# Kernel tuning notes

Measured on AMD Instinct MI355X. Metric: run time of the kernel, lower is better.

## Reference

```python
import jax, jax.numpy as jnp
import numpy as np

B, S, D = 4, 4096, 256


def _complex_linear(x_r, x_i, w_r, w_i):
    # torch nn.Linear: y = x @ W.T ; complex mult: (Wr + i Wi)(xr + i xi)
    real = x_r @ w_r.T - x_i @ w_i.T
    imag = x_i @ w_r.T + x_r @ w_i.T
    return real, imag


def setup_inputs() -> dict:
    key = jax.random.key(0)
    ks = jax.random.split(key, 8)
    std = 1.0 / np.sqrt(D)  # ~ nn.Linear default init scale
    return {
        "query_real": jax.random.normal(ks[0], (B, S, D), jnp.float32),
        "query_imag": jax.random.normal(ks[1], (B, S, D), jnp.float32),
        "wq_real": jax.random.normal(ks[2], (D, D), jnp.float32) * std,
        "wq_imag": jax.random.normal(ks[3], (D, D), jnp.float32) * std,
        "wk_real": jax.random.normal(ks[4], (D, D), jnp.float32) * std,
        "wk_imag": jax.random.normal(ks[5], (D, D), jnp.float32) * std,
        "wv_real": jax.random.normal(ks[6], (D, D), jnp.float32) * std,
        "wv_imag": jax.random.normal(ks[7], (D, D), jnp.float32) * std,
    }


def reference(query_real, query_imag, wq_real, wq_imag, wk_real, wk_imag, wv_real, wv_imag):
    dim = query_real.shape[-1]
    scale = dim ** (-0.5)  # faithful: uses dim, not 2*dim

    q_r, q_i = _complex_linear(query_real, query_imag, wq_real, wq_imag)
    k_r, k_i = _complex_linear(query_real, query_imag, wk_real, wk_imag)
    v_r, v_i = _complex_linear(query_real, query_imag, wv_real, wv_imag)

    q_flat = jnp.concatenate([q_r, q_i], axis=-1)  # [B,S,2D]
    k_flat = jnp.concatenate([k_r, k_i], axis=-1)  # [B,S,2D]

    scores = jnp.einsum('bqd,bkd->bqk', q_flat, k_flat) * scale  # [B,S,S]
    attn = jax.nn.softmax(scores, axis=-1)

    out_r = jnp.einsum('bqk,bkd->bqd', attn, v_r)
    out_i = jnp.einsum('bqk,bkd->bqd', attn, v_i)
    return out_r, out_i, attn
```

## Files before the change

### kernel.cpp

```cpp
#include <hip/hip_runtime.h>
#include <hip/hip_fp16.h>

typedef _Float16 f16;
typedef _Float16 f16x8 __attribute__((ext_vector_type(8)));
typedef _Float16 f16x4 __attribute__((ext_vector_type(4)));
typedef float f32x4 __attribute__((ext_vector_type(4)));

#define AS1 __attribute__((address_space(1)))
#define AS3 __attribute__((address_space(3)))

__device__ __forceinline__ void g2l16(const void* g, void* l) {
  __builtin_amdgcn_global_load_lds((const AS1 void*)g, (AS3 void*)l, 16, 0, 0);
}

__device__ __forceinline__ void xcd_swz(int& bx, int& by, int& bz) {
  int gx = gridDim.x, gy = gridDim.y;
  int nwg = gx * gy * gridDim.z;
  int lin = (blockIdx.z * gy + blockIdx.y) * gx + blockIdx.x;
  int swz = (lin & 7) * (nwg >> 3) + (lin >> 3);
  bx = swz % gx;
  int t = swz / gx;
  by = t % gy;
  bz = t / gy;
}

__global__ __launch_bounds__(256) void build_x(const float* __restrict__ qr,
                                               const float* __restrict__ qi,
                                               f16* __restrict__ X) {
  long i = (long)blockIdx.x * 256 + threadIdx.x;
  long e = i * 4;
  int m = (int)(e >> 9);
  int k = (int)(e & 511);
  const float* src = (k < 256) ? (qr + (long)m * 256 + k)
                               : (qi + (long)m * 256 + (k - 256));
  float4 v = *(const float4*)src;
  f16x4 h = {(f16)v.x, (f16)v.y, (f16)v.z, (f16)v.w};
  *(f16x4*)(X + e) = h;
}

__global__ __launch_bounds__(256) void build_w(const float* __restrict__ wqr,
                                               const float* __restrict__ wqi,
                                               const float* __restrict__ wkr,
                                               const float* __restrict__ wki,
                                               const float* __restrict__ wvr,
                                               const float* __restrict__ wvi,
                                               f16* __restrict__ W) {
  long i = (long)blockIdx.x * 256 + threadIdx.x;
  long e = i * 4;
  int n = (int)(e >> 9);
  int k = (int)(e & 511);
  int sel = n >> 8;
  int row = n & 255;
  int k2 = k & 255;
  bool hi = (k >= 256);
  const float *Wr, *Wi;
  if ((sel >> 1) == 0)      { Wr = wqr; Wi = wqi; }
  else if ((sel >> 1) == 1) { Wr = wkr; Wi = wki; }
  else                      { Wr = wvr; Wi = wvi; }
  const float* src;
  float sgn = 1.0f;
  if ((sel & 1) == 0) {
    if (!hi) src = Wr + (long)row * 256 + k2;
    else   { src = Wi + (long)row * 256 + k2; sgn = -1.0f; }
  } else {
    if (!hi) src = Wi + (long)row * 256 + k2;
    else     src = Wr + (long)row * 256 + k2;
  }
  float4 v = *(const float4*)src;
  f16x4 h = {(f16)(sgn * v.x), (f16)(sgn * v.y), (f16)(sgn * v.z), (f16)(sgn * v.w)};
  *(f16x4*)(W + e) = h;
}

template <int MODE>
__global__ __launch_bounds__(512, 4) void gemm_nt(const f16* __restrict__ A, int lda, long astr,
                                                  const f16* __restrict__ B, int ldb, long bstr,
                                                  int K, float scale,
                                                  void* __restrict__ C0, long cstr,
                                                  float2* __restrict__ stats) {
  __shared__ __align__(16) f16 As[256 * 64];
  __shared__ __align__(16) f16 Bs[128 * 64];
  int bx, by, bz;
  xcd_swz(bx, by, bz);
  const f16* Ab = A + (long)bz * astr;
  const f16* Bb = B + (long)bz * bstr;
  const int tid = threadIdx.x;
  const int wave = tid >> 6, lane = tid & 63;
  const int bm = by * 256, bn = bx * 128;
  const int wm = (wave >> 1) * 64, wn = (wave & 1) * 64;
  const int lr = lane & 15, lg = lane >> 4;

  const int srow = wave * 8 + (lane >> 3);
  const int sk = ((lane & 7) ^ (lane >> 3)) * 8;

  f32x4 acc[4][4] = {};

  for (int kt = 0; kt < K; kt += 64) {
#pragma unroll
    for (int it = 0; it < 4; ++it)
      g2l16(Ab + (long)(bm + srow + it * 64) * lda + kt + sk,
            (char*)As + it * 8192 + wave * 1024);
#pragma unroll
    for (int it = 0; it < 2; ++it)
      g2l16(Bb + (long)(bn + srow + it * 64) * ldb + kt + sk,
            (char*)Bs + it * 8192 + wave * 1024);
    __syncthreads();
#pragma unroll
    for (int kk = 0; kk < 2; ++kk) {
      f16x8 af[4], bf[4];
#pragma unroll
      for (int f = 0; f < 4; ++f) {
        int sw = ((kk * 4 + lg) ^ (lr & 7)) * 8;
        af[f] = *(const f16x8*)(As + (wm + f * 16 + lr) * 64 + sw);
        bf[f] = *(const f16x8*)(Bs + (wn + f * 16 + lr) * 64 + sw);
      }
#pragma unroll
      for (int fm = 0; fm < 4; ++fm)
#pragma unroll
        for (int fn = 0; fn < 4; ++fn)
          acc[fm][fn] = __builtin_amdgcn_mfma_f32_16x16x32_f16(af[fm], bf[fn], acc[fm][fn], 0, 0, 0);
    }
    __syncthreads();
  }

#pragma unroll
  for (int fm = 0; fm < 4; ++fm) {
#pragma unroll
    for (int fn = 0; fn < 4; ++fn) {
#pragma unroll
      for (int r = 0; r < 4; ++r) {
        int row = bm + wm + fm * 16 + lg * 4 + r;
        int col = bn + wn + fn * 16 + lr;
        float v = acc[fm][fn][r];
        if (MODE == 0) {
          ((f16*)C0)[(long)row * 1536 + col] = (f16)v;
        } else {
          ((f16*)C0)[(long)bz * cstr + (long)row * 4096 + col] = (f16)(v * scale);
        }
      }
    }
  }

  if (MODE == 1) {
    const int nt = bx * 2 + (wn >> 6);
#pragma unroll
    for (int fm = 0; fm < 4; ++fm) {
#pragma unroll
      for (int r = 0; r < 4; ++r) {
        float v0 = acc[fm][0][r] * scale, v1 = acc[fm][1][r] * scale;
        float v2 = acc[fm][2][r] * scale, v3 = acc[fm][3][r] * scale;
        float mt = fmaxf(fmaxf(v0, v1), fmaxf(v2, v3));
#pragma unroll
        for (int off = 8; off >= 1; off >>= 1) mt = fmaxf(mt, __shfl_xor(mt, off));
        float lt = __expf(v0 - mt) + __expf(v1 - mt) + __expf(v2 - mt) + __expf(v3 - mt);
#pragma unroll
        for (int off = 8; off >= 1; off >>= 1) lt += __shfl_xor(lt, off);
        if (lr == 0) {
          int row = bm + wm + fm * 16 + lg * 4 + r;
          stats[(long)nt * 16384 + (long)bz * 4096 + row] = make_float2(mt, lt);
        }
      }
    }
  }
}

__global__ __launch_bounds__(256) void build_vt(const f16* __restrict__ P,
                                                f16* __restrict__ VT) {
  __shared__ f16 t[64][66];
  const int tid = threadIdx.x;
  const long b = blockIdx.z;
  const f16* src = P + (b * 4096 + (long)blockIdx.x * 64) * 1536 + 1024 + blockIdx.y * 64;
#pragma unroll
  for (int it = 0; it < 16; ++it) {
    int lin = it * 256 + tid;
    int i = lin >> 6, j = lin & 63;
    t[i][j] = src[(long)i * 1536 + j];
  }
  __syncthreads();
  f16* dst = VT + (b * 512 + (long)blockIdx.y * 64) * 4096 + blockIdx.x * 64;
#pragma unroll
  for (int it = 0; it < 16; ++it) {
    int lin = it * 256 + tid;
    int i = lin >> 6, j = lin & 63;
    dst[(long)i * 4096 + j] = t[j][i];
  }
}

__global__ __launch_bounds__(256) void merge_stats(const float2* __restrict__ stats,
                                                   float2* __restrict__ ml) {
  long row = (long)blockIdx.x * 256 + threadIdx.x;
  float m = -1e30f;
#pragma unroll 8
  for (int i = 0; i < 64; ++i) m = fmaxf(m, stats[i * 16384 + row].x);
  float l = 0.0f;
#pragma unroll 8
  for (int i = 0; i < 64; ++i) {
    float2 s = stats[i * 16384 + row];
    l += s.y * __expf(s.x - m);
  }
  ml[row] = make_float2(m, l);
}

__global__ __launch_bounds__(512) void pv_fused4(const float2* __restrict__ ml,
                                                 const f16* __restrict__ S16,
                                                 const f16* __restrict__ VT,
                                                 float* __restrict__ attn,
                                                 float* __restrict__ outR,
                                                 float* __restrict__ outI) {
  __shared__ __align__(16) f16 Ps0[64 * 64];
  __shared__ __align__(16) f16 Ps1[64 * 64];
  __shared__ __align__(16) f16 Ps2[64 * 64];
  __shared__ __align__(16) f16 Bs0[256 * 64];
  __shared__ __align__(16) f16 Bs1[256 * 64];
  __shared__ __align__(16) f16 Bs2[256 * 64];
  int lin = blockIdx.x;
  int swz = (lin & 7) * 64 + (lin >> 3);
  int b = swz >> 7;
  int rem = swz & 127;
  int rt = rem >> 1, ch = rem & 1;
  const int bm = rt * 64;
  const int c0 = ch * 256;

  const int tid = threadIdx.x;
  const int wave = tid >> 6, lane = tid & 63;
  const int wm2 = (wave >> 2) * 32;
  const int wn2 = (wave & 3) * 64;
  const int lr = lane & 15, lg = lane >> 4;

  const int prow = tid >> 3;
  const int pc8 = tid & 7;
  const int vrow = wave * 8 + (lane >> 3);
  const int vsw = ((lane & 7) ^ ((lane >> 3) & 7)) * 8;
  float2 mlv = ml[(long)b * 4096 + bm + prow];
  const float mrow = mlv.x;
  const float invl = 1.0f / mlv.y;

  const f16* Sb = S16 + ((long)(b * 4096 + bm + prow)) * 4096 + pc8 * 8;
  float* Ab = attn + ((long)(b * 4096 + bm + prow)) * 4096 + pc8 * 8;
  const f16* Vb = VT + (long)(b * 512 + c0) * 4096;
  const int pslot = (pc8 ^ (prow & 7)) * 8;

  f32x4 acc[2][4] = {};
  f16x8 s0, s1, s2, sini;

#define PV_G2L(BSBUF, KT)                                                   \
  {                                                                         \
    _Pragma("unroll")                                                       \
    for (int i = 0; i < 4; ++i)                                             \
      g2l16(Vb + (long)(i * 64 + vrow) * 4096 + (KT) + vsw,                 \
            (char*)BSBUF + i * 8192 + wave * 1024);                         \
  }

#define PV_EXP(SC, PSBUF, KT, PAR)                                          \
  {                                                                         \
    float p[8];                                                             \
    _Pragma("unroll") for (int j = 0; j < 8; ++j)                           \
      p[j] = __expf((float)SC[j] - mrow) * invl;                            \
    if ((PAR) == ch) {                                                      \
      float4 w0 = {p[0], p[1], p[2], p[3]};                                 \
      float4 w1 = {p[4], p[5], p[6], p[7]};                                 \
      *(float4*)(Ab + (KT)) = w0;                                           \
      *(float4*)(Ab + (KT) + 4) = w1;                                       \
    }                                                                       \
    f16x8 h = {(f16)p[0], (f16)p[1], (f16)p[2], (f16)p[3],                  \
               (f16)p[4], (f16)p[5], (f16)p[6], (f16)p[7]};                 \
    *(f16x8*)(PSBUF + prow * 64 + pslot) = h;                               \
  }

#define PV_MFMA(PSBUF, BSBUF)                                               \
  {                                                                         \
    __builtin_amdgcn_s_setprio(1);                                          \
    _Pragma("unroll")                                                       \
    for (int kk = 0; kk < 2; ++kk) {                                        \
      f16x8 af[2];                                                          \
      _Pragma("unroll")                                                     \
      for (int fm = 0; fm < 2; ++fm)                                        \
        af[fm] = *(const f16x8*)(PSBUF + (wm2 + fm * 16 + lr) * 64 +        \
                                 ((kk * 4 + lg) ^ (lr & 7)) * 8);           \
      f16x8 bf[4];                                                          \
      _Pragma("unroll")                                                     \
      for (int f = 0; f < 4; ++f)                                           \
        bf[f] = *(const f16x8*)(BSBUF + (wn2 + f * 16 + lr) * 64 +          \
                                ((kk * 4 + lg) ^ (lr & 7)) * 8);            \
      _Pragma("unroll")                                                     \
      for (int fm = 0; fm < 2; ++fm)                                        \
        _Pragma("unroll")                                                   \
        for (int f = 0; f < 4; ++f)                                         \
          acc[fm][f] = __builtin_amdgcn_mfma_f32_16x16x32_f16(              \
              af[fm], bf[f], acc[fm][f], 0, 0, 0);                          \
    }                                                                       \
    __builtin_amdgcn_s_setprio(0);                                          \
  }

#define PV_SYNC(N)                                                          \
  asm volatile("s_waitcnt vmcnt(" #N ")" ::: "memory");                     \
  asm volatile("s_waitcnt lgkmcnt(0)" ::: "memory");                        \
  __builtin_amdgcn_s_barrier();                                             \
  __builtin_amdgcn_sched_barrier(0);

#define PV_TILE(T, BCUR, BPRE, PCUR, PNXT, SCONS, SLOAD)                    \
  {                                                                         \
    PV_G2L(BPRE, ((T) + 2) * 64)                                            \
    SLOAD = *(const f16x8*)(Sb + ((T) + 3) * 64);                           \
    PV_EXP(SCONS, PNXT, ((T) + 1) * 64, (((T) + 1) & 1))                    \
    PV_MFMA(PCUR, BCUR)                                                     \
    PV_SYNC(8)                                                              \
  }

  PV_G2L(Bs0, 0)
  PV_G2L(Bs1, 64)
  sini = *(const f16x8*)(Sb + 0);
  s1 = *(const f16x8*)(Sb + 64);
  s2 = *(const f16x8*)(Sb + 128);
  PV_EXP(sini, Ps0, 0, 0)
  PV_SYNC(7)

  for (int tb = 0; tb < 60; tb += 6) {
    PV_TILE(tb + 0, Bs0, Bs2, Ps0, Ps1, s1, s0)
    PV_TILE(tb + 1, Bs1, Bs0, Ps1, Ps2, s2, s1)
    PV_TILE(tb + 2, Bs2, Bs1, Ps2, Ps0, s0, s2)
    PV_TILE(tb + 3, Bs0, Bs2, Ps0, Ps1, s1, s0)
    PV_TILE(tb + 4, Bs1, Bs0, Ps1, Ps2, s2, s1)
    PV_TILE(tb + 5, Bs2, Bs1, Ps2, Ps0, s0, s2)
  }

  {
    PV_G2L(Bs2, 62 * 64)
    s0 = *(const f16x8*)(Sb + 63 * 64);
    PV_EXP(s1, Ps1, 61 * 64, 1)
    PV_MFMA(Ps0, Bs0)
    PV_SYNC(8)
  }
  {
    PV_G2L(Bs0, 63 * 64)
    PV_EXP(s2, Ps2, 62 * 64, 0)
    PV_MFMA(Ps1, Bs1)
    PV_SYNC(7)
  }
  {
    PV_EXP(s0, Ps0, 63 * 64, 1)
    PV_MFMA(Ps2, Bs2)
    PV_SYNC(2)
  }
  PV_MFMA(Ps0, Bs0)

#undef PV_TILE
#undef PV_SYNC
#undef PV_MFMA
#undef PV_EXP
#undef PV_G2L

  float* outp = ch ? outI : outR;
#pragma unroll
  for (int fm = 0; fm < 2; ++fm)
#pragma unroll
    for (int f = 0; f < 4; ++f)
#pragma unroll
      for (int r = 0; r < 4; ++r) {
        int row = bm + wm2 + fm * 16 + lg * 4 + r;
        int col = wn2 + f * 16 + lr;
        outp[((long)b * 4096 + row) * 256 + col] = acc[fm][f][r];
      }
}

extern "C" void kernel_launch(void* const* d_in, const int* in_sizes, int n_in,
                              void* d_out, int out_size, void* d_ws, size_t ws_size,
                              hipStream_t stream) {
  const float* qr  = (const float*)d_in[0];
  const float* qi  = (const float*)d_in[1];
  const float* wqr = (const float*)d_in[2];
  const float* wqi = (const float*)d_in[3];
  const float* wkr = (const float*)d_in[4];
  const float* wki = (const float*)d_in[5];
  const float* wvr = (const float*)d_in[6];
  const float* wvi = (const float*)d_in[7];

  float* outR = (float*)d_out;
  float* outI = outR + (size_t)4 * 4096 * 256;
  float* attn = outI + (size_t)4 * 4096 * 256;

  const size_t offX  = 0;
  const size_t offW  = offX + (size_t)16384 * 512 * 2;
  const size_t offP  = offW + (size_t)1536 * 512 * 2;
  const size_t offVT = offP + (size_t)16384 * 1536 * 2;
  const size_t offS  = offVT + (size_t)4 * 512 * 4096 * 2;

  char* ws = (char*)d_ws;
  f16* X   = (f16*)(ws + offX);
  f16* W   = (f16*)(ws + offW);
  f16* P   = (f16*)(ws + offP);
  f16* VT  = (f16*)(ws + offVT);
  f16* S16 = (f16*)(ws + offS);
  float2* stats = (float2*)X;
  float2* ml    = (float2*)W;

  build_x<<<8192, 256, 0, stream>>>(qr, qi, X);
  build_w<<<768, 256, 0, stream>>>(wqr, wqi, wkr, wki, wvr, wvi, W);

  gemm_nt<0><<<dim3(12, 64, 1), 512, 0, stream>>>(X, 512, 0L, W, 512, 0L, 512, 1.0f,
                                                  (void*)P, 0L, nullptr);

  build_vt<<<dim3(64, 8, 4), 256, 0, stream>>>(P, VT);

  gemm_nt<1><<<dim3(32, 16, 4), 512, 0, stream>>>(P, 1536, (long)4096 * 1536,
                                                  P + 512, 1536, (long)4096 * 1536,
                                                  512, 0.0625f,
                                                  (void*)S16, (long)4096 * 4096, stats);

  merge_stats<<<64, 256, 0, stream>>>(stats, ml);

  pv_fused4<<<512, 512, 0, stream>>>(ml, S16, VT, attn, outR, outI);
}
```

Before: 367.7 us.

## Compute softmax probabilities directly in MFMA A-fragment registers, skipping LDS staging

Replaces the PV kernel so each wave loads S16 scores straight into the register layout the MFMA A operand expects, exponentiates and normalizes them in registers, and feeds them to the MFMA without writing P into shared memory. Tiles become 128 rows by 128 output columns, with a double-buffered V tile in LDS and a launch bound hint for higher occupancy. Only the first column block writes the fp32 attention matrix, converting from the f16 fragments, so attn values now carry f16 rounding. This removes the LDS round trip and the P-tile barrier dependency, but each score is reloaded and exponentiated four times (once per column block) instead of twice.

```diff
diff --git a/kernel.cpp b/kernel.cpp
--- a/kernel.cpp
+++ b/kernel.cpp
@@ -200,166 +200,178 @@
   ml[row] = make_float2(m, l);
 }
 
-__global__ __launch_bounds__(512) void pv_fused4(const float2* __restrict__ ml,
-                                                 const f16* __restrict__ S16,
-                                                 const f16* __restrict__ VT,
-                                                 float* __restrict__ attn,
-                                                 float* __restrict__ outR,
-                                                 float* __restrict__ outI) {
-  __shared__ __align__(16) f16 Ps0[64 * 64];
-  __shared__ __align__(16) f16 Ps1[64 * 64];
-  __shared__ __align__(16) f16 Ps2[64 * 64];
-  __shared__ __align__(16) f16 Bs0[256 * 64];
-  __shared__ __align__(16) f16 Bs1[256 * 64];
-  __shared__ __align__(16) f16 Bs2[256 * 64];
+__global__ __launch_bounds__(512, 4) void pv_direct(const float2* __restrict__ ml,
+                                                    const f16* __restrict__ S16,
+                                                    const f16* __restrict__ VT,
+                                                    float* __restrict__ attn,
+                                                    float* __restrict__ outR,
+                                                    float* __restrict__ outI) {
+  __shared__ __align__(16) f16 Bs0[128 * 64];
+  __shared__ __align__(16) f16 Bs1[128 * 64];
   int lin = blockIdx.x;
   int swz = (lin & 7) * 64 + (lin >> 3);
+  int cb = swz & 3;
+  int rt = (swz >> 2) & 31;
   int b = swz >> 7;
-  int rem = swz & 127;
-  int rt = rem >> 1, ch = rem & 1;
-  const int bm = rt * 64;
-  const int c0 = ch * 256;
+  const int bm = rt * 128;
 
   const int tid = threadIdx.x;
   const int wave = tid >> 6, lane = tid & 63;
-  const int wm2 = (wave >> 2) * 32;
-  const int wn2 = (wave & 3) * 64;
+  const int wm3 = (wave >> 1) * 32;
+  const int wn3 = (wave & 1) * 64;
+  const int kkw = wave & 1;
   const int lr = lane & 15, lg = lane >> 4;
 
-  const int prow = tid >> 3;
-  const int pc8 = tid & 7;
   const int vrow = wave * 8 + (lane >> 3);
   const int vsw = ((lane & 7) ^ ((lane >> 3) & 7)) * 8;
-  float2 mlv = ml[(long)b * 4096 + bm + prow];
-  const float mrow = mlv.x;
-  const float invl = 1.0f / mlv.y;
-
-  const f16* Sb = S16 + ((long)(b * 4096 + bm + prow)) * 4096 + pc8 * 8;
-  float* Ab = attn + ((long)(b * 4096 + bm + prow)) * 4096 + pc8 * 8;
-  const f16* Vb = VT + (long)(b * 512 + c0) * 4096;
-  const int pslot = (pc8 ^ (prow & 7)) * 8;
+
+  float mrow[2], il[2];
+  {
+    float2 t0 = ml[(long)b * 4096 + bm + wm3 + lr];
+    float2 t1 = ml[(long)b * 4096 + bm + wm3 + 16 + lr];
+    mrow[0] = t0.x; il[0] = 1.0f / t0.y;
+    mrow[1] = t1.x; il[1] = 1.0f / t1.y;
+  }
+
+  const f16* Sfrag = S16 + ((long)(b * 4096 + bm + wm3 + lr)) * 4096 + lg * 8;
+  float* AbL = attn + ((long)(b * 4096 + bm + wm3 + lr)) * 4096 + lg * 8;
+  const f16* Vb = VT + (long)(b * 512 + cb * 128) * 4096;
 
   f32x4 acc[2][4] = {};
-  f16x8 s0, s1, s2, sini;
+  f16x8 frA[2][2], frB[2][2];
+  f16x8 af[2][2];
 
 #define PV_G2L(BSBUF, KT)                                                   \
   {                                                                         \
     _Pragma("unroll")                                                       \
-    for (int i = 0; i < 4; ++i)                                             \
+    for (int i = 0; i < 2; ++i)                                             \
       g2l16(Vb + (long)(i * 64 + vrow) * 4096 + (KT) + vsw,                 \
             (char*)BSBUF + i * 8192 + wave * 1024);                         \
   }
 
-#define PV_EXP(SC, PSBUF, KT, PAR)                                          \
-  {                                                                         \
-    float p[8];                                                             \
-    _Pragma("unroll") for (int j = 0; j < 8; ++j)                           \
-      p[j] = __expf((float)SC[j] - mrow) * invl;                            \
-    if ((PAR) == ch) {                                                      \
-      float4 w0 = {p[0], p[1], p[2], p[3]};                                 \
-      float4 w1 = {p[4], p[5], p[6], p[7]};                                 \
-      *(float4*)(Ab + (KT)) = w0;                                           \
-      *(float4*)(Ab + (KT) + 4) = w1;                                       \
-    }                                                                       \
-    f16x8 h = {(f16)p[0], (f16)p[1], (f16)p[2], (f16)p[3],                  \
-               (f16)p[4], (f16)p[5], (f16)p[6], (f16)p[7]};                 \
-    *(f16x8*)(PSBUF + prow * 64 + pslot) = h;                               \
-  }
-
-#define PV_MFMA(PSBUF, BSBUF)                                               \
+#define PV_FRAG(FR, T)                                                      \
+  {                                                                         \
+    _Pragma("unroll") for (int fm = 0; fm < 2; ++fm)                        \
+    _Pragma("unroll") for (int kk = 0; kk < 2; ++kk)                        \
+      FR[fm][kk] = *(const f16x8*)(Sfrag + (long)fm * 16 * 4096 +           \
+                                   (T) * 64 + kk * 32);                     \
+  }
+
+#define PV_MFMA(BSBUF)                                                      \
   {                                                                         \
     __builtin_amdgcn_s_setprio(1);                                          \
     _Pragma("unroll")                                                       \
     for (int kk = 0; kk < 2; ++kk) {                                        \
-      f16x8 af[2];                                                          \
-      _Pragma("unroll")                                                     \
-      for (int fm = 0; fm < 2; ++fm)                                        \
-        af[fm] = *(const f16x8*)(PSBUF + (wm2 + fm * 16 + lr) * 64 +        \
-                                 ((kk * 4 + lg) ^ (lr & 7)) * 8);           \
       f16x8 bf[4];                                                          \
       _Pragma("unroll")                                                     \
       for (int f = 0; f < 4; ++f)                                           \
-        bf[f] = *(const f16x8*)(BSBUF + (wn2 + f * 16 + lr) * 64 +          \
+        bf[f] = *(const f16x8*)(BSBUF + (wn3 + f * 16 + lr) * 64 +          \
                                 ((kk * 4 + lg) ^ (lr & 7)) * 8);            \
       _Pragma("unroll")                                                     \
       for (int fm = 0; fm < 2; ++fm)                                        \
         _Pragma("unroll")                                                   \
         for (int f = 0; f < 4; ++f)                                         \
           acc[fm][f] = __builtin_amdgcn_mfma_f32_16x16x32_f16(              \
-              af[fm], bf[f], acc[fm][f], 0, 0, 0);                          \
+              af[fm][kk], bf[f], acc[fm][f], 0, 0, 0);                      \
     }                                                                       \
     __builtin_amdgcn_s_setprio(0);                                          \
   }
 
-#define PV_SYNC(N)                                                          \
+#define PV_STORES(T, DOST)                                                  \
+  if (DOST) {                                                               \
+    _Pragma("unroll")                                                       \
+    for (int fm = 0; fm < 2; ++fm) {                                        \
+      f16x8 v = af[fm][kkw];                                                \
+      float4 w0 = {(float)v[0], (float)v[1], (float)v[2], (float)v[3]};     \
+      float4 w1 = {(float)v[4], (float)v[5], (float)v[6], (float)v[7]};     \
+      float* dst = AbL + (long)fm * 16 * 4096 + (T) * 64 + kkw * 32;        \
+      *(float4*)dst = w0;                                                   \
+      *(float4*)(dst + 4) = w1;                                             \
+    }                                                                       \
+  }
+
+#define PV_EXP(FR)                                                          \
+  {                                                                         \
+    _Pragma("unroll") for (int fm = 0; fm < 2; ++fm)                        \
+    _Pragma("unroll") for (int kk = 0; kk < 2; ++kk) {                      \
+      f16x8 h;                                                              \
+      _Pragma("unroll") for (int j = 0; j < 8; ++j)                         \
+        h[j] = (f16)(__expf((float)FR[fm][kk][j] - mrow[fm]) * il[fm]);     \
+      af[fm][kk] = h;                                                       \
+    }                                                                       \
+  }
+
+#define PV_SYNC_(N)                                                         \
   asm volatile("s_waitcnt vmcnt(" #N ")" ::: "memory");                     \
   asm volatile("s_waitcnt lgkmcnt(0)" ::: "memory");                        \
   __builtin_amdgcn_s_barrier();                                             \
   __builtin_amdgcn_sched_barrier(0);
-
-#define PV_TILE(T, BCUR, BPRE, PCUR, PNXT, SCONS, SLOAD)                    \
-  {                                                                         \
-    PV_G2L(BPRE, ((T) + 2) * 64)                                            \
-    SLOAD = *(const f16x8*)(Sb + ((T) + 3) * 64);                           \
-    PV_EXP(SCONS, PNXT, ((T) + 1) * 64, (((T) + 1) & 1))                    \
-    PV_MFMA(PCUR, BCUR)                                                     \
-    PV_SYNC(8)                                                              \
-  }
-
-  PV_G2L(Bs0, 0)
-  PV_G2L(Bs1, 64)
-  sini = *(const f16x8*)(Sb + 0);
-  s1 = *(const f16x8*)(Sb + 64);
-  s2 = *(const f16x8*)(Sb + 128);
-  PV_EXP(sini, Ps0, 0, 0)
-  PV_SYNC(7)
-
-  for (int tb = 0; tb < 60; tb += 6) {
-    PV_TILE(tb + 0, Bs0, Bs2, Ps0, Ps1, s1, s0)
-    PV_TILE(tb + 1, Bs1, Bs0, Ps1, Ps2, s2, s1)
-    PV_TILE(tb + 2, Bs2, Bs1, Ps2, Ps0, s0, s2)
-    PV_TILE(tb + 3, Bs0, Bs2, Ps0, Ps1, s1, s0)
-    PV_TILE(tb + 4, Bs1, Bs0, Ps1, Ps2, s2, s1)
-    PV_TILE(tb + 5, Bs2, Bs1, Ps2, Ps0, s0, s2)
-  }
-
-  {
-    PV_G2L(Bs2, 62 * 64)
-    s0 = *(const f16x8*)(Sb + 63 * 64);
-    PV_EXP(s1, Ps1, 61 * 64, 1)
-    PV_MFMA(Ps0, Bs0)
-    PV_SYNC(8)
-  }
-  {
-    PV_G2L(Bs0, 63 * 64)
-    PV_EXP(s2, Ps2, 62 * 64, 0)
-    PV_MFMA(Ps1, Bs1)
-    PV_SYNC(7)
-  }
-  {
-    PV_EXP(s0, Ps0, 63 * 64, 1)
-    PV_MFMA(Ps2, Bs2)
-    PV_SYNC(2)
-  }
-  PV_MFMA(Ps0, Bs0)
-
+#define PV_SYNC(N) PV_SYNC_(N)
+
+#define PV_TILE(T, BCUR, BNXT, FRLD, FRCONS, VMN, DOST)                     \
+  {                                                                         \
+    PV_G2L(BNXT, ((T) + 1) * 64)                                            \
+    PV_FRAG(FRLD, (T) + 2)                                                  \
+    PV_MFMA(BCUR)                                                           \
+    PV_STORES(T, DOST)                                                      \
+    PV_EXP(FRCONS)                                                          \
+    PV_SYNC(VMN)                                                            \
+  }
+
+#define PV_RUN(VMF, VME, DOST)                                              \
+  {                                                                         \
+              \
+    PV_G2L(Bs0, 0)                                                          \
+    PV_FRAG(frA, 0)                                                         \
+    PV_FRAG(frB, 1)                                                         \
+    PV_SYNC(4)                                                              \
+    PV_EXP(frA)                                                             \
+    for (int t = 0; t < 62; t += 2) {                                       \
+      PV_TILE(t, Bs0, Bs1, frA, frB, VMF, DOST)                             \
+      PV_TILE(t + 1, Bs1, Bs0, frB, frA, VMF, DOST)                         \
+    }                                                                       \
+                                                   \
+    {                                                                       \
+      PV_G2L(Bs1, 63 * 64)                                                  \
+      PV_MFMA(Bs0)                                                          \
+      PV_STORES(62, DOST)                                                   \
+      PV_EXP(frB)                                                           \
+      PV_SYNC(VME)                                                          \
+    }                                                                       \
+                                                                \
+    PV_MFMA(Bs1)                                                            \
+    PV_STORES(63, DOST)                                                     \
+  }
+
+  if (cb == 0) {
+    PV_RUN(8, 4, 1)
+  } else {
+    PV_RUN(4, 0, 0)
+  }
+
+#undef PV_RUN
 #undef PV_TILE
 #undef PV_SYNC
+#undef PV_SYNC_
+#undef PV_EXP
+#undef PV_STORES
 #undef PV_MFMA
-#undef PV_EXP
+#undef PV_FRAG
 #undef PV_G2L
 
-  float* outp = ch ? outI : outR;
-#pragma unroll
-  for (int fm = 0; fm < 2; ++fm)
-#pragma unroll
-    for (int f = 0; f < 4; ++f)
+#pragma unroll
+  for (int fm = 0; fm < 2; ++fm) {
+#pragma unroll
+    for (int fn = 0; fn < 4; ++fn) {
 #pragma unroll
       for (int r = 0; r < 4; ++r) {
-        int row = bm + wm2 + fm * 16 + lg * 4 + r;
-        int col = wn2 + f * 16 + lr;
-        outp[((long)b * 4096 + row) * 256 + col] = acc[fm][f][r];
+        int row = bm + wm3 + fm * 16 + lg * 4 + r;
+        int col = cb * 128 + wn3 + fn * 16 + lr;
+        float* outp = (col < 256) ? outR : outI;
+        outp[((long)b * 4096 + row) * 256 + (col & 255)] = acc[fm][fn][r];
       }
+    }
+  }
 }
 
 extern "C" void kernel_launch(void* const* d_in, const int* in_sizes, int n_in,
@@ -408,5 +420,5 @@
 
   merge_stats<<<64, 256, 0, stream>>>(stats, ml);
 
-  pv_fused4<<<512, 512, 0, stream>>>(ml, S16, VT, attn, outR, outI);
-}
+  pv_direct<<<512, 512, 0, stream>>>(ml, S16, VT, attn, outR, outI);
+}
```

Measured after the change: 1.381 ms. 276% more time.

## Switch PV kernel to double-buffering and split attn-store ownership per block

Applied to the files above, without the earlier changes.

The fused P·V kernel goes from a triple-buffered LDS pipeline with prefetch distance two to double buffers with distance one. This cuts LDS per block roughly by a third, and launch bounds are added to allow more resident blocks. The attn store now belongs entirely to the ch==0 block instead of alternating tiles between the two channel blocks. Each specialised path gets its own vmcnt wait values. Less latency hiding per block and an uneven store load between the two block types are the risks traded for higher occupancy.

```diff
diff --git a/kernel.cpp b/kernel.cpp
--- a/kernel.cpp
+++ b/kernel.cpp
@@ -200,18 +200,16 @@
   ml[row] = make_float2(m, l);
 }
 
-__global__ __launch_bounds__(512) void pv_fused4(const float2* __restrict__ ml,
-                                                 const f16* __restrict__ S16,
-                                                 const f16* __restrict__ VT,
-                                                 float* __restrict__ attn,
-                                                 float* __restrict__ outR,
-                                                 float* __restrict__ outI) {
+__global__ __launch_bounds__(512, 4) void pv_fused5(const float2* __restrict__ ml,
+                                                    const f16* __restrict__ S16,
+                                                    const f16* __restrict__ VT,
+                                                    float* __restrict__ attn,
+                                                    float* __restrict__ outR,
+                                                    float* __restrict__ outI) {
   __shared__ __align__(16) f16 Ps0[64 * 64];
   __shared__ __align__(16) f16 Ps1[64 * 64];
-  __shared__ __align__(16) f16 Ps2[64 * 64];
   __shared__ __align__(16) f16 Bs0[256 * 64];
   __shared__ __align__(16) f16 Bs1[256 * 64];
-  __shared__ __align__(16) f16 Bs2[256 * 64];
   int lin = blockIdx.x;
   int swz = (lin & 7) * 64 + (lin >> 3);
   int b = swz >> 7;
@@ -240,7 +238,7 @@
   const int pslot = (pc8 ^ (prow & 7)) * 8;
 
   f32x4 acc[2][4] = {};
-  f16x8 s0, s1, s2, sini;
+  f16x8 scA, scB;
 
 #define PV_G2L(BSBUF, KT)                                                   \
   {                                                                         \
@@ -250,12 +248,12 @@
             (char*)BSBUF + i * 8192 + wave * 1024);                         \
   }
 
-#define PV_EXP(SC, PSBUF, KT, PAR)                                          \
+#define PV_EXP(SC, PSBUF, KT, DOST)                                         \
   {                                                                         \
     float p[8];                                                             \
     _Pragma("unroll") for (int j = 0; j < 8; ++j)                           \
       p[j] = __expf((float)SC[j] - mrow) * invl;                            \
-    if ((PAR) == ch) {                                                      \
+    if (DOST) {                                                             \
       float4 w0 = {p[0], p[1], p[2], p[3]};                                 \
       float4 w1 = {p[4], p[5], p[6], p[7]};                                 \
       *(float4*)(Ab + (KT)) = w0;                                           \
@@ -291,60 +289,55 @@
     __builtin_amdgcn_s_setprio(0);                                          \
   }
 
-#define PV_SYNC(N)                                                          \
+#define PV_SYNC_(N)                                                         \
   asm volatile("s_waitcnt vmcnt(" #N ")" ::: "memory");                     \
   asm volatile("s_waitcnt lgkmcnt(0)" ::: "memory");                        \
   __builtin_amdgcn_s_barrier();                                             \
   __builtin_amdgcn_sched_barrier(0);
-
-#define PV_TILE(T, BCUR, BPRE, PCUR, PNXT, SCONS, SLOAD)                    \
+#define PV_SYNC(N) PV_SYNC_(N)
+
+#define PV_TILE(T, BCUR, BNXT, PCUR, PNXT, SCONS, SLOAD, VMN, DOST)         \
   {                                                                         \
-    PV_G2L(BPRE, ((T) + 2) * 64)                                            \
-    SLOAD = *(const f16x8*)(Sb + ((T) + 3) * 64);                           \
-    PV_EXP(SCONS, PNXT, ((T) + 1) * 64, (((T) + 1) & 1))                    \
+    PV_G2L(BNXT, ((T) + 1) * 64)                                            \
+    SLOAD = *(const f16x8*)(Sb + ((T) + 2) * 64);                           \
     PV_MFMA(PCUR, BCUR)                                                     \
-    PV_SYNC(8)                                                              \
-  }
-
-  PV_G2L(Bs0, 0)
-  PV_G2L(Bs1, 64)
-  sini = *(const f16x8*)(Sb + 0);
-  s1 = *(const f16x8*)(Sb + 64);
-  s2 = *(const f16x8*)(Sb + 128);
-  PV_EXP(sini, Ps0, 0, 0)
-  PV_SYNC(7)
-
-  for (int tb = 0; tb < 60; tb += 6) {
-    PV_TILE(tb + 0, Bs0, Bs2, Ps0, Ps1, s1, s0)
-    PV_TILE(tb + 1, Bs1, Bs0, Ps1, Ps2, s2, s1)
-    PV_TILE(tb + 2, Bs2, Bs1, Ps2, Ps0, s0, s2)
-    PV_TILE(tb + 3, Bs0, Bs2, Ps0, Ps1, s1, s0)
-    PV_TILE(tb + 4, Bs1, Bs0, Ps1, Ps2, s2, s1)
-    PV_TILE(tb + 5, Bs2, Bs1, Ps2, Ps0, s0, s2)
-  }
-
-  {
-    PV_G2L(Bs2, 62 * 64)
-    s0 = *(const f16x8*)(Sb + 63 * 64);
-    PV_EXP(s1, Ps1, 61 * 64, 1)
-    PV_MFMA(Ps0, Bs0)
-    PV_SYNC(8)
-  }
-  {
-    PV_G2L(Bs0, 63 * 64)
-    PV_EXP(s2, Ps2, 62 * 64, 0)
-    PV_MFMA(Ps1, Bs1)
-    PV_SYNC(7)
-  }
-  {
-    PV_EXP(s0, Ps0, 63 * 64, 1)
-    PV_MFMA(Ps2, Bs2)
-    PV_SYNC(2)
-  }
-  PV_MFMA(Ps0, Bs0)
-
+    PV_EXP(SCONS, PNXT, ((T) + 1) * 64, DOST)                               \
+    PV_SYNC(VMN)                                                            \
+  }
+
+#define PV_RUN(VMF, VMP, VME, DOST)                                         \
+  {                                                                         \
+                   \
+    PV_G2L(Bs0, 0)                                                          \
+    scA = *(const f16x8*)(Sb + 0);                                          \
+    scB = *(const f16x8*)(Sb + 64);                                         \
+    PV_EXP(scA, Ps0, 0, DOST)                                               \
+    PV_SYNC(VMP)                                                            \
+    for (int t = 0; t < 62; t += 2) {                                       \
+      PV_TILE(t, Bs0, Bs1, Ps0, Ps1, scB, scA, VMF, DOST)                   \
+      PV_TILE(t + 1, Bs1, Bs0, Ps1, Ps0, scA, scB, VMF, DOST)               \
+    }                                                                       \
+                                        \
+    {                                                                       \
+      PV_G2L(Bs1, 63 * 64)                                                  \
+      PV_MFMA(Ps0, Bs0)                                                     \
+      PV_EXP(scB, Ps1, 63 * 64, DOST)                                       \
+      PV_SYNC(VME)                                                          \
+    }                                                                       \
+                                                               \
+    PV_MFMA(Ps1, Bs1)                                                       \
+  }
+
+  if (ch == 0) {
+    PV_RUN(3, 3, 2, 1)
+  } else {
+    PV_RUN(1, 1, 0, 0)
+  }
+
+#undef PV_RUN
 #undef PV_TILE
 #undef PV_SYNC
+#undef PV_SYNC_
 #undef PV_MFMA
 #undef PV_EXP
 #undef PV_G2L
@@ -408,5 +401,5 @@
 
   merge_stats<<<64, 256, 0, stream>>>(stats, ml);
 
-  pv_fused4<<<512, 512, 0, stream>>>(ml, S16, VT, attn, outR, outI);
-}
+  pv_fused5<<<512, 512, 0, stream>>>(ml, S16, VT, attn, outR, outI);
+}
```

After: 350.6 us. -4.6%, faster.
